# Kernel tuning notes

Hardware: AMD Instinct MI355X
Metric: run time of the kernel (lower is better)

## Reference

```python
import jax, jax.numpy as jnp
import numpy as np

MAX_DEPTH = 10
NUM_INPUT = 256
NUM_OUTPUT = 64
BATCH = 131072
N_INTERNAL = 2**MAX_DEPTH - 1  # 1023 heap-indexed internal nodes
N_LEAVES = 2**MAX_DEPTH        # 1024 leaves


def setup_inputs() -> dict:
    key = jax.random.key(0)
    k_x, k_w, k_b, k_a, k_l = jax.random.split(key, 5)
    x = jax.random.normal(k_x, (BATCH, NUM_INPUT), dtype=jnp.float32)
    # internal-node params (torch init: weights ~ N(0,0.1); bias/alpha zeros,
    # but we randomize bias/alpha so both branches are exercised)
    W = jax.random.normal(k_w, (N_INTERNAL, NUM_INPUT), dtype=jnp.float32) * 0.1
    b = jax.random.normal(k_b, (N_INTERNAL,), dtype=jnp.float32) * 0.1
    alpha = jax.random.normal(k_a, (N_INTERNAL,), dtype=jnp.float32)
    leaves = jax.random.normal(k_l, (N_LEAVES, NUM_OUTPUT), dtype=jnp.float32)
    return {"x": x, "W": W, "b": b, "alpha": alpha, "leaves": leaves}


def reference(x, W, b, alpha, leaves):
    # Batched hard root-to-leaf traversal of the soft binary tree.
    # Heap indexing: node i -> left child 2i+1, right child 2i+2.
    B = x.shape[0]
    idx = jnp.zeros((B,), dtype=jnp.int32)
    mult = jnp.ones((B,), dtype=x.dtype)
    for _ in range(MAX_DEPTH):  # fixed small structural loop over depth levels
        w = W[idx]  # [B, F] gather of per-node weights
        val = jax.nn.sigmoid(alpha[idx] * (jnp.einsum('bf,bf->b', x, w) + b[idx]))
        go_right = val >= 0.5
        # right branch contributes val, left branch contributes (1 - val)
        mult = mult * jnp.where(go_right, val, 1.0 - val)
        idx = 2 * idx + 1 + go_right.astype(jnp.int32)
    leaf_idx = idx - N_INTERNAL  # [B]
    return mult[:, None] * leaves[leaf_idx]  # [B, num_output]
```

## Files before the change

kernel.cpp:

```cpp
#include <hip/hip_runtime.h>

#define NUM_INPUT   256
#define NUM_OUTPUT  64
#define MAX_DEPTH   10
#define N_INTERNAL  1023
#define STAGED_NODES 31
#define STAGED_DEPTH 5
#define ELEMS_PER_WAVE 4
#define WAVES_PER_BLOCK 8
#define THREADS (WAVES_PER_BLOCK * 64)
#define ELEMS_PER_BLOCK (WAVES_PER_BLOCK * ELEMS_PER_WAVE)

__device__ __forceinline__ float group16_reduce_add(float acc) {
    int t;
    t = __builtin_amdgcn_update_dpp(0, __float_as_int(acc), 0x121, 0xf, 0xf, true);
    acc += __int_as_float(t);
    t = __builtin_amdgcn_update_dpp(0, __float_as_int(acc), 0x122, 0xf, 0xf, true);
    acc += __int_as_float(t);
    t = __builtin_amdgcn_update_dpp(0, __float_as_int(acc), 0x124, 0xf, 0xf, true);
    acc += __int_as_float(t);
    t = __builtin_amdgcn_update_dpp(0, __float_as_int(acc), 0x128, 0xf, 0xf, true);
    acc += __int_as_float(t);
    return acc;
}

__device__ __forceinline__ float group16_reduce_mul(float v) {
    int t;
    t = __builtin_amdgcn_update_dpp(0, __float_as_int(v), 0x121, 0xf, 0xf, true);
    v *= __int_as_float(t);
    t = __builtin_amdgcn_update_dpp(0, __float_as_int(v), 0x122, 0xf, 0xf, true);
    v *= __int_as_float(t);
    t = __builtin_amdgcn_update_dpp(0, __float_as_int(v), 0x124, 0xf, 0xf, true);
    v *= __int_as_float(t);
    t = __builtin_amdgcn_update_dpp(0, __float_as_int(v), 0x128, 0xf, 0xf, true);
    v *= __int_as_float(t);
    return v;
}

__global__ __launch_bounds__(THREADS, 8) void ogtree_kernel(
    const float* __restrict__ x,
    const float* __restrict__ W,
    const float* __restrict__ b,
    const float* __restrict__ alpha,
    const float* __restrict__ leaves,
    float* __restrict__ out)
{
    __shared__ float lds_w[STAGED_NODES * NUM_INPUT];
    __shared__ float lds_b[N_INTERNAL];
    __shared__ float lds_a[N_INTERNAL];

    const int tid  = threadIdx.x;
    const int lane = tid & 63;
    const int wid  = tid >> 6;
    const int g    = lane >> 4;
    const int s    = lane & 15;
    const int elem = blockIdx.x * ELEMS_PER_BLOCK + wid * ELEMS_PER_WAVE + g;

    const float4* xrow = reinterpret_cast<const float4*>(x + (size_t)elem * NUM_INPUT);
    float4 xv0 = xrow[0 * 16 + s];
    float4 xv1 = xrow[1 * 16 + s];
    float4 xv2 = xrow[2 * 16 + s];
    float4 xv3 = xrow[3 * 16 + s];

    {
        const float4* Wv = reinterpret_cast<const float4*>(W);
        float4* lw4 = reinterpret_cast<float4*>(lds_w);
        #pragma unroll
        for (int i = tid; i < STAGED_NODES * NUM_INPUT / 4; i += THREADS)
            lw4[i] = Wv[i];
        for (int i = tid; i < N_INTERNAL; i += THREADS) {
            lds_b[i] = b[i];
            lds_a[i] = alpha[i];
        }
    }
    __syncthreads();

    int   idx = 0;
    float zn[MAX_DEPTH];

    #define DEPTH_STEP(BASE, D)                                            \
    {                                                                      \
        const float4* wrow = reinterpret_cast<const float4*>(              \
            (BASE) + (size_t)idx * NUM_INPUT);                             \
        float a_i = lds_a[idx];                                            \
        float b_i = lds_b[idx];                                            \
        float4 w0 = wrow[0 * 16 + s];                                      \
        float4 w1 = wrow[1 * 16 + s];                                      \
        float4 w2 = wrow[2 * 16 + s];                                      \
        float4 w3 = wrow[3 * 16 + s];                                      \
        float acc0 = xv0.x * w0.x, acc1 = xv1.x * w1.x;                    \
        float acc2 = xv2.x * w2.x, acc3 = xv3.x * w3.x;                    \
        acc0 = fmaf(xv0.y, w0.y, acc0); acc1 = fmaf(xv1.y, w1.y, acc1);    \
        acc2 = fmaf(xv2.y, w2.y, acc2); acc3 = fmaf(xv3.y, w3.y, acc3);    \
        acc0 = fmaf(xv0.z, w0.z, acc0); acc1 = fmaf(xv1.z, w1.z, acc1);    \
        acc2 = fmaf(xv2.z, w2.z, acc2); acc3 = fmaf(xv3.z, w3.z, acc3);    \
        acc0 = fmaf(xv0.w, w0.w, acc0); acc1 = fmaf(xv1.w, w1.w, acc1);    \
        acc2 = fmaf(xv2.w, w2.w, acc2); acc3 = fmaf(xv3.w, w3.w, acc3);    \
        float acc = (acc0 + acc1) + (acc2 + acc3);                         \
        acc = group16_reduce_add(acc);                                     \
        float z = a_i * (acc + b_i);                                       \
        zn[D] = __int_as_float(__float_as_int(z) | 0x80000000);  \
        bool right = (z >= 0.0f);                                          \
        idx = 2 * idx + 1 + (right ? 1 : 0);                               \
    }

    #pragma unroll
    for (int d = 0; d < STAGED_DEPTH; ++d)
        DEPTH_STEP(lds_w, d);
    #pragma unroll
    for (int d = STAGED_DEPTH; d < MAX_DEPTH; ++d)
        DEPTH_STEP(W, d);
    #undef DEPTH_STEP

    float zsel = -1e30f;
    #pragma unroll
    for (int d = 0; d < MAX_DEPTH; ++d)
        zsel = (s == d) ? zn[d] : zsel;
    float f = 1.0f + __expf(zsel);
    float p = group16_reduce_mul(f);
    float mult = 1.0f / p;

    const int leaf = idx - N_INTERNAL;
    const float4 lv = reinterpret_cast<const float4*>(
        leaves + (size_t)leaf * NUM_OUTPUT)[s];
    float4 o;
    o.x = mult * lv.x;
    o.y = mult * lv.y;
    o.z = mult * lv.z;
    o.w = mult * lv.w;
    reinterpret_cast<float4*>(out + (size_t)elem * NUM_OUTPUT)[s] = o;
}

extern "C" void kernel_launch(void* const* d_in, const int* in_sizes, int n_in,
                              void* d_out, int out_size, void* d_ws, size_t ws_size,
                              hipStream_t stream) {
    const float* x      = (const float*)d_in[0];
    const float* W      = (const float*)d_in[1];
    const float* b      = (const float*)d_in[2];
    const float* alpha  = (const float*)d_in[3];
    const float* leaves = (const float*)d_in[4];
    float* out = (float*)d_out;

    const int batch  = in_sizes[0] / NUM_INPUT;
    const int blocks = batch / ELEMS_PER_BLOCK;

    ogtree_kernel<<<blocks, THREADS, 0, stream>>>(x, W, b, alpha, leaves, out);
}
```

Before: 49.42 us.

## Prefetch both child weight rows speculatively to hide global load latency

The global-memory depth levels now load the weight rows of both children of the current node while the current dot product is computed, then pick the correct one once the branch decision is known. The leaf rows for both final candidates are also fetched before the last decision. This takes the dependent global load off the critical path of each level, at the cost of twice the weight traffic and more registers. To make room for those registers the occupancy hint in launch bounds drops from 8 to 4.

```diff
diff --git a/kernel.cpp b/kernel.cpp
--- a/kernel.cpp
+++ b/kernel.cpp
@@ -37,7 +37,16 @@
     return v;
 }
 
-__global__ __launch_bounds__(THREADS, 8) void ogtree_kernel(
+__device__ __forceinline__ float4 sel4(bool c, float4 r, float4 l) {
+    float4 o;
+    o.x = c ? r.x : l.x;
+    o.y = c ? r.y : l.y;
+    o.z = c ? r.z : l.z;
+    o.w = c ? r.w : l.w;
+    return o;
+}
+
+__global__ __launch_bounds__(THREADS, 4) void ogtree_kernel(
     const float* __restrict__ x,
     const float* __restrict__ W,
     const float* __restrict__ b,
@@ -76,12 +85,13 @@
     __syncthreads();
 
     int   idx = 0;
+    bool  right;
     float zn[MAX_DEPTH];
 
-    #define DEPTH_STEP(BASE, D)                                            \
+    #define LDS_STEP(D)                                                    \
     {                                                                      \
         const float4* wrow = reinterpret_cast<const float4*>(              \
-            (BASE) + (size_t)idx * NUM_INPUT);                             \
+            lds_w + idx * NUM_INPUT);                                      \
         float a_i = lds_a[idx];                                            \
         float b_i = lds_b[idx];                                            \
         float4 w0 = wrow[0 * 16 + s];                                      \
@@ -100,17 +110,111 @@
         acc = group16_reduce_add(acc);                                     \
         float z = a_i * (acc + b_i);                                       \
         zn[D] = __int_as_float(__float_as_int(z) | 0x80000000);  \
-        bool right = (z >= 0.0f);                                          \
+        right = (z >= 0.0f);                                               \
         idx = 2 * idx + 1 + (right ? 1 : 0);                               \
     }
 
-    #pragma unroll
-    for (int d = 0; d < STAGED_DEPTH; ++d)
-        DEPTH_STEP(lds_w, d);
-    #pragma unroll
-    for (int d = STAGED_DEPTH; d < MAX_DEPTH; ++d)
-        DEPTH_STEP(W, d);
-    #undef DEPTH_STEP
+    LDS_STEP(0)
+    LDS_STEP(1)
+    LDS_STEP(2)
+    LDS_STEP(3)
+    #undef LDS_STEP
+
+    float4 wL0, wL1, wL2, wL3, wR0, wR1, wR2, wR3;
+
+    {
+        const float4* wrow = reinterpret_cast<const float4*>(lds_w + idx * NUM_INPUT);
+        float a_i = lds_a[idx];
+        float b_i = lds_b[idx];
+        float4 w0 = wrow[0 * 16 + s];
+        float4 w1 = wrow[1 * 16 + s];
+        float4 w2 = wrow[2 * 16 + s];
+        float4 w3 = wrow[3 * 16 + s];
+        const float4* pL = reinterpret_cast<const float4*>(W + (size_t)(2 * idx + 1) * NUM_INPUT);
+        const float4* pR = reinterpret_cast<const float4*>(W + (size_t)(2 * idx + 2) * NUM_INPUT);
+        wL0 = pL[0 * 16 + s]; wL1 = pL[1 * 16 + s];
+        wL2 = pL[2 * 16 + s]; wL3 = pL[3 * 16 + s];
+        wR0 = pR[0 * 16 + s]; wR1 = pR[1 * 16 + s];
+        wR2 = pR[2 * 16 + s]; wR3 = pR[3 * 16 + s];
+        float acc0 = xv0.x * w0.x, acc1 = xv1.x * w1.x;
+        float acc2 = xv2.x * w2.x, acc3 = xv3.x * w3.x;
+        acc0 = fmaf(xv0.y, w0.y, acc0); acc1 = fmaf(xv1.y, w1.y, acc1);
+        acc2 = fmaf(xv2.y, w2.y, acc2); acc3 = fmaf(xv3.y, w3.y, acc3);
+        acc0 = fmaf(xv0.z, w0.z, acc0); acc1 = fmaf(xv1.z, w1.z, acc1);
+        acc2 = fmaf(xv2.z, w2.z, acc2); acc3 = fmaf(xv3.z, w3.z, acc3);
+        acc0 = fmaf(xv0.w, w0.w, acc0); acc1 = fmaf(xv1.w, w1.w, acc1);
+        acc2 = fmaf(xv2.w, w2.w, acc2); acc3 = fmaf(xv3.w, w3.w, acc3);
+        float acc = (acc0 + acc1) + (acc2 + acc3);
+        acc = group16_reduce_add(acc);
+        float z = a_i * (acc + b_i);
+        zn[4] = __int_as_float(__float_as_int(z) | 0x80000000);
+        right = (z >= 0.0f);
+        idx = 2 * idx + 1 + (right ? 1 : 0);
+    }
+
+    #define GSTEP(D)                                                       \
+    {                                                                      \
+        float4 w0 = sel4(right, wR0, wL0);                                 \
+        float4 w1 = sel4(right, wR1, wL1);                                 \
+        float4 w2 = sel4(right, wR2, wL2);                                 \
+        float4 w3 = sel4(right, wR3, wL3);                                 \
+        float a_i = lds_a[idx];                                            \
+        float b_i = lds_b[idx];                                            \
+        const float4* pL = reinterpret_cast<const float4*>(                \
+            W + (size_t)(2 * idx + 1) * NUM_INPUT);                        \
+        const float4* pR = reinterpret_cast<const float4*>(                \
+            W + (size_t)(2 * idx + 2) * NUM_INPUT);                        \
+        wL0 = pL[0 * 16 + s]; wL1 = pL[1 * 16 + s];                        \
+        wL2 = pL[2 * 16 + s]; wL3 = pL[3 * 16 + s];                        \
+        wR0 = pR[0 * 16 + s]; wR1 = pR[1 * 16 + s];                        \
+        wR2 = pR[2 * 16 + s]; wR3 = pR[3 * 16 + s];                        \
+        float acc0 = xv0.x * w0.x, acc1 = xv1.x * w1.x;                    \
+        float acc2 = xv2.x * w2.x, acc3 = xv3.x * w3.x;                    \
+        acc0 = fmaf(xv0.y, w0.y, acc0); acc1 = fmaf(xv1.y, w1.y, acc1);    \
+        acc2 = fmaf(xv2.y, w2.y, acc2); acc3 = fmaf(xv3.y, w3.y, acc3);    \
+        acc0 = fmaf(xv0.z, w0.z, acc0); acc1 = fmaf(xv1.z, w1.z, acc1);    \
+        acc2 = fmaf(xv2.z, w2.z, acc2); acc3 = fmaf(xv3.z, w3.z, acc3);    \
+        acc0 = fmaf(xv0.w, w0.w, acc0); acc1 = fmaf(xv1.w, w1.w, acc1);    \
+        acc2 = fmaf(xv2.w, w2.w, acc2); acc3 = fmaf(xv3.w, w3.w, acc3);    \
+        float acc = (acc0 + acc1) + (acc2 + acc3);                         \
+        acc = group16_reduce_add(acc);                                     \
+        float z = a_i * (acc + b_i);                                       \
+        zn[D] = __int_as_float(__float_as_int(z) | 0x80000000);            \
+        right = (z >= 0.0f);                                               \
+        idx = 2 * idx + 1 + (right ? 1 : 0);                               \
+    }
+
+    GSTEP(5)
+    GSTEP(6)
+    GSTEP(7)
+    GSTEP(8)
+    #undef GSTEP
+
+    float4 lvL, lvR;
+    {
+        float4 w0 = sel4(right, wR0, wL0);
+        float4 w1 = sel4(right, wR1, wL1);
+        float4 w2 = sel4(right, wR2, wL2);
+        float4 w3 = sel4(right, wR3, wL3);
+        float a_i = lds_a[idx];
+        float b_i = lds_b[idx];
+        const int leafL = 2 * idx + 1 - N_INTERNAL;
+        lvL = reinterpret_cast<const float4*>(leaves + (size_t)leafL * NUM_OUTPUT)[s];
+        lvR = reinterpret_cast<const float4*>(leaves + (size_t)(leafL + 1) * NUM_OUTPUT)[s];
+        float acc0 = xv0.x * w0.x, acc1 = xv1.x * w1.x;
+        float acc2 = xv2.x * w2.x, acc3 = xv3.x * w3.x;
+        acc0 = fmaf(xv0.y, w0.y, acc0); acc1 = fmaf(xv1.y, w1.y, acc1);
+        acc2 = fmaf(xv2.y, w2.y, acc2); acc3 = fmaf(xv3.y, w3.y, acc3);
+        acc0 = fmaf(xv0.z, w0.z, acc0); acc1 = fmaf(xv1.z, w1.z, acc1);
+        acc2 = fmaf(xv2.z, w2.z, acc2); acc3 = fmaf(xv3.z, w3.z, acc3);
+        acc0 = fmaf(xv0.w, w0.w, acc0); acc1 = fmaf(xv1.w, w1.w, acc1);
+        acc2 = fmaf(xv2.w, w2.w, acc2); acc3 = fmaf(xv3.w, w3.w, acc3);
+        float acc = (acc0 + acc1) + (acc2 + acc3);
+        acc = group16_reduce_add(acc);
+        float z = a_i * (acc + b_i);
+        zn[9] = __int_as_float(__float_as_int(z) | 0x80000000);
+        right = (z >= 0.0f);
+    }
 
     float zsel = -1e30f;
     #pragma unroll
@@ -120,9 +224,7 @@
     float p = group16_reduce_mul(f);
     float mult = 1.0f / p;
 
-    const int leaf = idx - N_INTERNAL;
-    const float4 lv = reinterpret_cast<const float4*>(
-        leaves + (size_t)leaf * NUM_OUTPUT)[s];
+    const float4 lv = sel4(right, lvR, lvL);
     float4 o;
     o.x = mult * lv.x;
     o.y = mult * lv.y;
```

After: 66.02 us. +33.6%, slower.

## Split traversal into two phases with bucket sort by depth-5 node

Applied to the files above, without the earlier changes.

Splits the single traversal kernel into a pipeline. A first pass walks the top five levels from LDS and records each element's depth-5 node and partial product. Elements are then counting-sorted into 32 buckets by that node, and a second pass stages each bucket's 31-node subtree of W into LDS so the bottom five levels read from shared memory instead of gathering from global memory. In exchange it adds five kernel launches, rereads x a second time, and adds indirect scattered writes. A fallback monolithic kernel runs when the workspace is too small.

```diff
diff --git a/kernel.cpp b/kernel.cpp
--- a/kernel.cpp
+++ b/kernel.cpp
@@ -4,12 +4,7 @@
 #define NUM_OUTPUT  64
 #define MAX_DEPTH   10
 #define N_INTERNAL  1023
-#define STAGED_NODES 31
-#define STAGED_DEPTH 5
-#define ELEMS_PER_WAVE 4
-#define WAVES_PER_BLOCK 8
-#define THREADS (WAVES_PER_BLOCK * 64)
-#define ELEMS_PER_BLOCK (WAVES_PER_BLOCK * ELEMS_PER_WAVE)
+
 
 __device__ __forceinline__ float group16_reduce_add(float acc) {
     int t;
@@ -37,80 +32,240 @@
     return v;
 }
 
-__global__ __launch_bounds__(THREADS, 8) void ogtree_kernel(
-    const float* __restrict__ x,
-    const float* __restrict__ W,
-    const float* __restrict__ b,
-    const float* __restrict__ alpha,
-    const float* __restrict__ leaves,
-    float* __restrict__ out)
-{
-    __shared__ float lds_w[STAGED_NODES * NUM_INPUT];
-    __shared__ float lds_b[N_INTERNAL];
-    __shared__ float lds_a[N_INTERNAL];
+#define DOT16(WPTR, ACC)                                                    \
+    {                                                                       \
+        const float4* wr_ = reinterpret_cast<const float4*>(WPTR);          \
+        float4 w0 = wr_[s], w1 = wr_[16 + s], w2 = wr_[32 + s], w3 = wr_[48 + s]; \
+        float a0 = xv0.x * w0.x, a1 = xv1.x * w1.x;                         \
+        float a2 = xv2.x * w2.x, a3 = xv3.x * w3.x;                         \
+        a0 = fmaf(xv0.y, w0.y, a0); a1 = fmaf(xv1.y, w1.y, a1);             \
+        a2 = fmaf(xv2.y, w2.y, a2); a3 = fmaf(xv3.y, w3.y, a3);             \
+        a0 = fmaf(xv0.z, w0.z, a0); a1 = fmaf(xv1.z, w1.z, a1);             \
+        a2 = fmaf(xv2.z, w2.z, a2); a3 = fmaf(xv3.z, w3.z, a3);             \
+        a0 = fmaf(xv0.w, w0.w, a0); a1 = fmaf(xv1.w, w1.w, a1);             \
+        a2 = fmaf(xv2.w, w2.w, a2); a3 = fmaf(xv3.w, w3.w, a3);             \
+        ACC = group16_reduce_add((a0 + a1) + (a2 + a3));                    \
+    }
+
+#define TREE_STEP(WBASE, AARR, BARR, IDX, ZND)                              \
+    {                                                                       \
+        float a_i = (AARR)[IDX];                                            \
+        float b_i = (BARR)[IDX];                                            \
+        float acc_;                                                         \
+        DOT16((WBASE) + (size_t)(IDX) * NUM_INPUT, acc_);                   \
+        float z = a_i * (acc_ + b_i);                                       \
+        ZND = __int_as_float(__float_as_int(z) | 0x80000000);               \
+        IDX = 2 * (IDX) + 1 + ((z >= 0.0f) ? 1 : 0);                        \
+    }
+
+#define P1_THREADS 1024
+#define P1_ELEMS   64
+
+__global__ __launch_bounds__(P1_THREADS) void ogtree_p1(
+    const float* __restrict__ x, const float* __restrict__ W,
+    const float* __restrict__ b, const float* __restrict__ alpha,
+    int* __restrict__ cnt, int* __restrict__ idx5a, float* __restrict__ p5a)
+{
+    __shared__ float lds_w[31 * NUM_INPUT];
+    __shared__ float la[31], lb_[31];
+    __shared__ int   h[32];
 
     const int tid  = threadIdx.x;
-    const int lane = tid & 63;
-    const int wid  = tid >> 6;
-    const int g    = lane >> 4;
-    const int s    = lane & 15;
-    const int elem = blockIdx.x * ELEMS_PER_BLOCK + wid * ELEMS_PER_WAVE + g;
+    const int lane = tid & 63, wid = tid >> 6;
+    const int g    = lane >> 4, s = lane & 15;
+    const int elem = blockIdx.x * P1_ELEMS + wid * 4 + g;
 
     const float4* xrow = reinterpret_cast<const float4*>(x + (size_t)elem * NUM_INPUT);
-    float4 xv0 = xrow[0 * 16 + s];
-    float4 xv1 = xrow[1 * 16 + s];
-    float4 xv2 = xrow[2 * 16 + s];
-    float4 xv3 = xrow[3 * 16 + s];
+    float4 xv0 = xrow[s], xv1 = xrow[16 + s], xv2 = xrow[32 + s], xv3 = xrow[48 + s];
 
     {
         const float4* Wv = reinterpret_cast<const float4*>(W);
         float4* lw4 = reinterpret_cast<float4*>(lds_w);
         #pragma unroll
-        for (int i = tid; i < STAGED_NODES * NUM_INPUT / 4; i += THREADS)
-            lw4[i] = Wv[i];
-        for (int i = tid; i < N_INTERNAL; i += THREADS) {
-            lds_b[i] = b[i];
-            lds_a[i] = alpha[i];
+        for (int i = tid; i < 31 * 64; i += P1_THREADS) lw4[i] = Wv[i];
+        if (tid < 31) { la[tid] = alpha[tid]; lb_[tid] = b[tid]; }
+        if (tid < 32) h[tid] = 0;
+    }
+    __syncthreads();
+
+    int idx = 0;
+    float zn[5];
+    #pragma unroll
+    for (int d = 0; d < 5; ++d)
+        TREE_STEP(lds_w, la, lb_, idx, zn[d]);
+
+    float zsel = -1e30f;
+    #pragma unroll
+    for (int d = 0; d < 5; ++d)
+        zsel = (s == d) ? zn[d] : zsel;
+    float f = 1.0f + __expf(zsel);
+    float p = group16_reduce_mul(f);
+
+    if (s == 0) {
+        idx5a[elem] = idx;
+        p5a[elem]   = p;
+        atomicAdd(&h[idx - 31], 1);
+    }
+    __syncthreads();
+    if (tid < 32 && h[tid] > 0) atomicAdd(&cnt[tid], h[tid]);
+}
+
+__global__ void ogtree_scan(const int* __restrict__ cnt, int* __restrict__ cur)
+{
+    if (threadIdx.x == 0) {
+        int acc = 0;
+        for (int i = 0; i < 32; ++i) { cur[i] = acc; acc += cnt[i]; }
+    }
+}
+
+__global__ void ogtree_zero(int* __restrict__ cnt)
+{
+    if (threadIdx.x < 32) cnt[threadIdx.x] = 0;
+}
+
+#define SC_THREADS 256
+__global__ __launch_bounds__(SC_THREADS) void ogtree_scatter(
+    const int* __restrict__ idx5a, int* __restrict__ cur, int* __restrict__ ids)
+{
+    __shared__ int h[32], base[32];
+    const int tid = threadIdx.x;
+    const int e   = blockIdx.x * SC_THREADS + tid;
+    if (tid < 32) h[tid] = 0;
+    __syncthreads();
+    const int bkt  = idx5a[e] - 31;
+    const int rank = atomicAdd(&h[bkt], 1);
+    __syncthreads();
+    if (tid < 32 && h[tid] > 0) base[tid] = atomicAdd(&cur[tid], h[tid]);
+    __syncthreads();
+    ids[base[bkt] + rank] = e;
+}
+
+#define P2_THREADS 1024
+#define P2_ELEMS   64
+
+__global__ __launch_bounds__(P2_THREADS) void ogtree_p2(
+    const float* __restrict__ x, const float* __restrict__ W,
+    const float* __restrict__ b, const float* __restrict__ alpha,
+    const float* __restrict__ leaves,
+    const int* __restrict__ ids, const int* __restrict__ idx5a,
+    const float* __restrict__ p5a, float* __restrict__ out)
+{
+    __shared__ float lsub[31 * NUM_INPUT];
+    __shared__ float la[31], lb_[31];
+    __shared__ int   s_n5, s_uni;
+
+    const int tid  = threadIdx.x;
+    const int lane = tid & 63, wid = tid >> 6;
+    const int g    = lane >> 4, s = lane & 15;
+    const int i0   = blockIdx.x * P2_ELEMS;
+
+    const int   id   = ids[i0 + wid * 4 + g];
+    const int   myn5 = idx5a[id];
+    const float p5v  = p5a[id];
+
+    const float4* xrow = reinterpret_cast<const float4*>(x + (size_t)id * NUM_INPUT);
+    float4 xv0 = xrow[s], xv1 = xrow[16 + s], xv2 = xrow[32 + s], xv3 = xrow[48 + s];
+
+    if (tid == 0) {
+        int na = idx5a[ids[i0]];
+        int nb = idx5a[ids[i0 + P2_ELEMS - 1]];
+        s_n5  = na;
+        s_uni = (na == nb);
+    }
+    __syncthreads();
+    const bool uni = (s_uni != 0);
+    const int  n5  = s_n5;
+
+    if (uni) {
+        const float4* Wv = reinterpret_cast<const float4*>(W);
+        float4* ls4 = reinterpret_cast<float4*>(lsub);
+        #pragma unroll
+        for (int i = tid; i < 31 * 64; i += P2_THREADS) {
+            int row = i >> 6;
+            int col = i & 63;
+            int lvl = 31 - __clz(row + 1);
+            int gl  = ((n5 + 1) << lvl) - 1 + (row + 1 - (1 << lvl));
+            ls4[row * 64 + col] = Wv[(size_t)gl * 64 + col];
         }
-    }
-    __syncthreads();
-
-    int   idx = 0;
+        if (tid < 31) {
+            int lvl = 31 - __clz(tid + 1);
+            int gl  = ((n5 + 1) << lvl) - 1 + (tid + 1 - (1 << lvl));
+            la[tid]  = alpha[gl];
+            lb_[tid] = b[gl];
+        }
+    }
+    __syncthreads();
+
+    float zn[5];
+    int leaf;
+    if (uni) {
+        int li = 0;
+        #pragma unroll
+        for (int d = 0; d < 5; ++d)
+            TREE_STEP(lsub, la, lb_, li, zn[d]);
+        leaf = (((n5 + 1) << 5) - 1 + (li - 31)) - N_INTERNAL;
+    } else {
+        int idxg = myn5;
+        #pragma unroll
+        for (int d = 0; d < 5; ++d)
+            TREE_STEP(W, alpha, b, idxg, zn[d]);
+        leaf = idxg - N_INTERNAL;
+    }
+
+    float zsel = -1e30f;
+    #pragma unroll
+    for (int d = 0; d < 5; ++d)
+        zsel = (s == d) ? zn[d] : zsel;
+    float f = 1.0f + __expf(zsel);
+    float p = group16_reduce_mul(f);
+    float mult = 1.0f / (p * p5v);
+
+    const float4 lv = reinterpret_cast<const float4*>(
+        leaves + (size_t)leaf * NUM_OUTPUT)[s];
+    float4 o;
+    o.x = mult * lv.x;
+    o.y = mult * lv.y;
+    o.z = mult * lv.z;
+    o.w = mult * lv.w;
+    reinterpret_cast<float4*>(out + (size_t)id * NUM_OUTPUT)[s] = o;
+}
+
+#define MONO_THREADS 512
+#define MONO_ELEMS   32
+
+__global__ __launch_bounds__(MONO_THREADS) void ogtree_mono(
+    const float* __restrict__ x, const float* __restrict__ W,
+    const float* __restrict__ b, const float* __restrict__ alpha,
+    const float* __restrict__ leaves, float* __restrict__ out)
+{
+    __shared__ float lds_w[31 * NUM_INPUT];
+    __shared__ float la[31], lb_[31];
+
+    const int tid  = threadIdx.x;
+    const int lane = tid & 63, wid = tid >> 6;
+    const int g    = lane >> 4, s = lane & 15;
+    const int elem = blockIdx.x * MONO_ELEMS + wid * 4 + g;
+
+    const float4* xrow = reinterpret_cast<const float4*>(x + (size_t)elem * NUM_INPUT);
+    float4 xv0 = xrow[s], xv1 = xrow[16 + s], xv2 = xrow[32 + s], xv3 = xrow[48 + s];
+
+    {
+        const float4* Wv = reinterpret_cast<const float4*>(W);
+        float4* lw4 = reinterpret_cast<float4*>(lds_w);
+        #pragma unroll
+        for (int i = tid; i < 31 * 64; i += MONO_THREADS) lw4[i] = Wv[i];
+        if (tid < 31) { la[tid] = alpha[tid]; lb_[tid] = b[tid]; }
+    }
+    __syncthreads();
+
+    int idx = 0;
     float zn[MAX_DEPTH];
-
-    #define DEPTH_STEP(BASE, D)                                            \
-    {                                                                      \
-        const float4* wrow = reinterpret_cast<const float4*>(              \
-            (BASE) + (size_t)idx * NUM_INPUT);                             \
-        float a_i = lds_a[idx];                                            \
-        float b_i = lds_b[idx];                                            \
-        float4 w0 = wrow[0 * 16 + s];                                      \
-        float4 w1 = wrow[1 * 16 + s];                                      \
-        float4 w2 = wrow[2 * 16 + s];                                      \
-        float4 w3 = wrow[3 * 16 + s];                                      \
-        float acc0 = xv0.x * w0.x, acc1 = xv1.x * w1.x;                    \
-        float acc2 = xv2.x * w2.x, acc3 = xv3.x * w3.x;                    \
-        acc0 = fmaf(xv0.y, w0.y, acc0); acc1 = fmaf(xv1.y, w1.y, acc1);    \
-        acc2 = fmaf(xv2.y, w2.y, acc2); acc3 = fmaf(xv3.y, w3.y, acc3);    \
-        acc0 = fmaf(xv0.z, w0.z, acc0); acc1 = fmaf(xv1.z, w1.z, acc1);    \
-        acc2 = fmaf(xv2.z, w2.z, acc2); acc3 = fmaf(xv3.z, w3.z, acc3);    \
-        acc0 = fmaf(xv0.w, w0.w, acc0); acc1 = fmaf(xv1.w, w1.w, acc1);    \
-        acc2 = fmaf(xv2.w, w2.w, acc2); acc3 = fmaf(xv3.w, w3.w, acc3);    \
-        float acc = (acc0 + acc1) + (acc2 + acc3);                         \
-        acc = group16_reduce_add(acc);                                     \
-        float z = a_i * (acc + b_i);                                       \
-        zn[D] = __int_as_float(__float_as_int(z) | 0x80000000);  \
-        bool right = (z >= 0.0f);                                          \
-        idx = 2 * idx + 1 + (right ? 1 : 0);                               \
-    }
-
-    #pragma unroll
-    for (int d = 0; d < STAGED_DEPTH; ++d)
-        DEPTH_STEP(lds_w, d);
-    #pragma unroll
-    for (int d = STAGED_DEPTH; d < MAX_DEPTH; ++d)
-        DEPTH_STEP(W, d);
-    #undef DEPTH_STEP
+    #pragma unroll
+    for (int d = 0; d < 5; ++d)
+        TREE_STEP(lds_w, la, lb_, idx, zn[d]);
+    #pragma unroll
+    for (int d = 5; d < MAX_DEPTH; ++d)
+        TREE_STEP(W, alpha, b, idx, zn[d]);
 
     float zsel = -1e30f;
     #pragma unroll
@@ -141,8 +296,26 @@
     const float* leaves = (const float*)d_in[4];
     float* out = (float*)d_out;
 
-    const int batch  = in_sizes[0] / NUM_INPUT;
-    const int blocks = batch / ELEMS_PER_BLOCK;
-
-    ogtree_kernel<<<blocks, THREADS, 0, stream>>>(x, W, b, alpha, leaves, out);
-}
+    const int batch = in_sizes[0] / NUM_INPUT;
+
+    const size_t need = 64 * sizeof(int) + (size_t)batch * 4 * 3;
+    if (ws_size < need) {
+        ogtree_mono<<<batch / MONO_ELEMS, MONO_THREADS, 0, stream>>>(
+            x, W, b, alpha, leaves, out);
+        return;
+    }
+
+    int*   cnt   = (int*)d_ws;
+    int*   cur   = cnt + 32;
+    int*   idx5a = cnt + 64;
+    float* p5a   = (float*)(idx5a + batch);
+    int*   ids   = (int*)(p5a + batch);
+
+    ogtree_zero<<<1, 64, 0, stream>>>(cnt);
+    ogtree_p1<<<batch / P1_ELEMS, P1_THREADS, 0, stream>>>(
+        x, W, b, alpha, cnt, idx5a, p5a);
+    ogtree_scan<<<1, 64, 0, stream>>>(cnt, cur);
+    ogtree_scatter<<<batch / SC_THREADS, SC_THREADS, 0, stream>>>(idx5a, cur, ids);
+    ogtree_p2<<<batch / P2_ELEMS, P2_THREADS, 0, stream>>>(
+        x, W, b, alpha, leaves, ids, idx5a, p5a, out);
+}
```

Result: slower. 91.44 us (+85.0%).

## Process four elements per group with software-prefetched x rows

Applied to the files above, without the earlier changes.

Each 16-lane group now handles four batch elements in sequence instead of one. The grid shrinks to a fixed 1024 blocks, so the LDS staging of the top tree levels is amortised over more elements. The next element's x row is prefetched into a second register set while the global-memory levels of the current element run, hiding load latency. This adds register pressure (launch bounds lowered to 4 waves/SIMD) and hardcodes the grid size to the test batch.

```diff
diff --git a/kernel.cpp b/kernel.cpp
--- a/kernel.cpp
+++ b/kernel.cpp
@@ -5,11 +5,9 @@
 #define MAX_DEPTH   10
 #define N_INTERNAL  1023
 #define STAGED_NODES 31
-#define STAGED_DEPTH 5
-#define ELEMS_PER_WAVE 4
-#define WAVES_PER_BLOCK 8
-#define THREADS (WAVES_PER_BLOCK * 64)
-#define ELEMS_PER_BLOCK (WAVES_PER_BLOCK * ELEMS_PER_WAVE)
+#define THREADS 512
+#define NBLOCKS 1024
+#define ELEMS_PER_GROUP 4
 
 __device__ __forceinline__ float group16_reduce_add(float acc) {
     int t;
@@ -37,7 +35,71 @@
     return v;
 }
 
-__global__ __launch_bounds__(THREADS, 8) void ogtree_kernel(
+#define STEP_X(BASE, IDX, ZND, X0, X1, X2, X3)                              \
+    {                                                                       \
+        float a_i = lds_a[IDX];                                             \
+        float b_i = lds_b[IDX];                                             \
+        const float4* wr_ = reinterpret_cast<const float4*>(                \
+            (BASE) + (size_t)(IDX) * NUM_INPUT);                            \
+        float4 w0 = wr_[s], w1 = wr_[16 + s], w2 = wr_[32 + s], w3 = wr_[48 + s]; \
+        float a0 = X0.x * w0.x, a1 = X1.x * w1.x;                           \
+        float a2 = X2.x * w2.x, a3 = X3.x * w3.x;                           \
+        a0 = fmaf(X0.y, w0.y, a0); a1 = fmaf(X1.y, w1.y, a1);               \
+        a2 = fmaf(X2.y, w2.y, a2); a3 = fmaf(X3.y, w3.y, a3);               \
+        a0 = fmaf(X0.z, w0.z, a0); a1 = fmaf(X1.z, w1.z, a1);               \
+        a2 = fmaf(X2.z, w2.z, a2); a3 = fmaf(X3.z, w3.z, a3);               \
+        a0 = fmaf(X0.w, w0.w, a0); a1 = fmaf(X1.w, w1.w, a1);               \
+        a2 = fmaf(X2.w, w2.w, a2); a3 = fmaf(X3.w, w3.w, a3);               \
+        float acc_ = group16_reduce_add((a0 + a1) + (a2 + a3));             \
+        float z = a_i * (acc_ + b_i);                                       \
+        ZND = __int_as_float(__float_as_int(z) | 0x80000000);               \
+        IDX = 2 * (IDX) + 1 + ((z >= 0.0f) ? 1 : 0);                        \
+    }
+
+#define ONE_ELEM(E, XC0, XC1, XC2, XC3, XN0, XN1, XN2, XN3, PF)             \
+    {                                                                       \
+        int idx = 0;                                                        \
+        float zn0, zn1, zn2, zn3, zn4, zn5, zn6, zn7, zn8, zn9;             \
+                                        \
+        STEP_X(lds_w, idx, zn0, XC0, XC1, XC2, XC3)                         \
+        STEP_X(lds_w, idx, zn1, XC0, XC1, XC2, XC3)                         \
+        STEP_X(lds_w, idx, zn2, XC0, XC1, XC2, XC3)                         \
+        STEP_X(lds_w, idx, zn3, XC0, XC1, XC2, XC3)                         \
+        STEP_X(lds_w, idx, zn4, XC0, XC1, XC2, XC3)                         \
+        if (PF) {                                                           \
+            const float4* xp_ = reinterpret_cast<const float4*>(            \
+                x + (size_t)(gbase + 4 * ((E) + 1)) * NUM_INPUT);           \
+            XN0 = xp_[s];      XN1 = xp_[16 + s];                           \
+            XN2 = xp_[32 + s]; XN3 = xp_[48 + s];                           \
+            __builtin_amdgcn_sched_barrier(0);                              \
+        }                                                                   \
+           \
+        STEP_X(W, idx, zn5, XC0, XC1, XC2, XC3)                             \
+        STEP_X(W, idx, zn6, XC0, XC1, XC2, XC3)                             \
+        STEP_X(W, idx, zn7, XC0, XC1, XC2, XC3)                             \
+        STEP_X(W, idx, zn8, XC0, XC1, XC2, XC3)                             \
+        STEP_X(W, idx, zn9, XC0, XC1, XC2, XC3)                             \
+                 \
+        float zsel = -1e30f;                                                \
+        zsel = (s == 0) ? zn0 : zsel; zsel = (s == 1) ? zn1 : zsel;         \
+        zsel = (s == 2) ? zn2 : zsel; zsel = (s == 3) ? zn3 : zsel;         \
+        zsel = (s == 4) ? zn4 : zsel; zsel = (s == 5) ? zn5 : zsel;         \
+        zsel = (s == 6) ? zn6 : zsel; zsel = (s == 7) ? zn7 : zsel;         \
+        zsel = (s == 8) ? zn8 : zsel; zsel = (s == 9) ? zn9 : zsel;         \
+        float f = 1.0f + __expf(zsel);                                      \
+        float p = group16_reduce_mul(f);                                    \
+        float mult = 1.0f / p;                                              \
+        const int leaf = idx - N_INTERNAL;                                  \
+        const float4 lv = reinterpret_cast<const float4*>(                  \
+            leaves + (size_t)leaf * NUM_OUTPUT)[s];                         \
+        float4 o;                                                           \
+        o.x = mult * lv.x; o.y = mult * lv.y;                               \
+        o.z = mult * lv.z; o.w = mult * lv.w;                               \
+        reinterpret_cast<float4*>(                                          \
+            out + (size_t)(gbase + 4 * (E)) * NUM_OUTPUT)[s] = o;           \
+    }
+
+__global__ __launch_bounds__(THREADS, 4) void ogtree_kernel(
     const float* __restrict__ x,
     const float* __restrict__ W,
     const float* __restrict__ b,
@@ -54,13 +116,10 @@
     const int wid  = tid >> 6;
     const int g    = lane >> 4;
     const int s    = lane & 15;
-    const int elem = blockIdx.x * ELEMS_PER_BLOCK + wid * ELEMS_PER_WAVE + g;
+    const int gbase = blockIdx.x * (THREADS / 64) * 16 + wid * 16 + g;
 
-    const float4* xrow = reinterpret_cast<const float4*>(x + (size_t)elem * NUM_INPUT);
-    float4 xv0 = xrow[0 * 16 + s];
-    float4 xv1 = xrow[1 * 16 + s];
-    float4 xv2 = xrow[2 * 16 + s];
-    float4 xv3 = xrow[3 * 16 + s];
+    const float4* xp0 = reinterpret_cast<const float4*>(x + (size_t)gbase * NUM_INPUT);
+    float4 xa0 = xp0[s], xa1 = xp0[16 + s], xa2 = xp0[32 + s], xa3 = xp0[48 + s];
 
     {
         const float4* Wv = reinterpret_cast<const float4*>(W);
@@ -75,60 +134,12 @@
     }
     __syncthreads();
 
-    int   idx = 0;
-    float zn[MAX_DEPTH];
+    float4 xb0, xb1, xb2, xb3;
 
-    #define DEPTH_STEP(BASE, D)                                            \
-    {                                                                      \
-        const float4* wrow = reinterpret_cast<const float4*>(              \
-            (BASE) + (size_t)idx * NUM_INPUT);                             \
-        float a_i = lds_a[idx];                                            \
-        float b_i = lds_b[idx];                                            \
-        float4 w0 = wrow[0 * 16 + s];                                      \
-        float4 w1 = wrow[1 * 16 + s];                                      \
-        float4 w2 = wrow[2 * 16 + s];                                      \
-        float4 w3 = wrow[3 * 16 + s];                                      \
-        float acc0 = xv0.x * w0.x, acc1 = xv1.x * w1.x;                    \
-        float acc2 = xv2.x * w2.x, acc3 = xv3.x * w3.x;                    \
-        acc0 = fmaf(xv0.y, w0.y, acc0); acc1 = fmaf(xv1.y, w1.y, acc1);    \
-        acc2 = fmaf(xv2.y, w2.y, acc2); acc3 = fmaf(xv3.y, w3.y, acc3);    \
-        acc0 = fmaf(xv0.z, w0.z, acc0); acc1 = fmaf(xv1.z, w1.z, acc1);    \
-        acc2 = fmaf(xv2.z, w2.z, acc2); acc3 = fmaf(xv3.z, w3.z, acc3);    \
-        acc0 = fmaf(xv0.w, w0.w, acc0); acc1 = fmaf(xv1.w, w1.w, acc1);    \
-        acc2 = fmaf(xv2.w, w2.w, acc2); acc3 = fmaf(xv3.w, w3.w, acc3);    \
-        float acc = (acc0 + acc1) + (acc2 + acc3);                         \
-        acc = group16_reduce_add(acc);                                     \
-        float z = a_i * (acc + b_i);                                       \
-        zn[D] = __int_as_float(__float_as_int(z) | 0x80000000);  \
-        bool right = (z >= 0.0f);                                          \
-        idx = 2 * idx + 1 + (right ? 1 : 0);                               \
-    }
-
-    #pragma unroll
-    for (int d = 0; d < STAGED_DEPTH; ++d)
-        DEPTH_STEP(lds_w, d);
-    #pragma unroll
-    for (int d = STAGED_DEPTH; d < MAX_DEPTH; ++d)
-        DEPTH_STEP(W, d);
-    #undef DEPTH_STEP
-
-    float zsel = -1e30f;
-    #pragma unroll
-    for (int d = 0; d < MAX_DEPTH; ++d)
-        zsel = (s == d) ? zn[d] : zsel;
-    float f = 1.0f + __expf(zsel);
-    float p = group16_reduce_mul(f);
-    float mult = 1.0f / p;
-
-    const int leaf = idx - N_INTERNAL;
-    const float4 lv = reinterpret_cast<const float4*>(
-        leaves + (size_t)leaf * NUM_OUTPUT)[s];
-    float4 o;
-    o.x = mult * lv.x;
-    o.y = mult * lv.y;
-    o.z = mult * lv.z;
-    o.w = mult * lv.w;
-    reinterpret_cast<float4*>(out + (size_t)elem * NUM_OUTPUT)[s] = o;
+    ONE_ELEM(0, xa0, xa1, xa2, xa3, xb0, xb1, xb2, xb3, 1)
+    ONE_ELEM(1, xb0, xb1, xb2, xb3, xa0, xa1, xa2, xa3, 1)
+    ONE_ELEM(2, xa0, xa1, xa2, xa3, xb0, xb1, xb2, xb3, 1)
+    ONE_ELEM(3, xb0, xb1, xb2, xb3, xa0, xa1, xa2, xa3, 0)
 }
 
 extern "C" void kernel_launch(void* const* d_in, const int* in_sizes, int n_in,
@@ -141,8 +152,5 @@
     const float* leaves = (const float*)d_in[4];
     float* out = (float*)d_out;
 
-    const int batch  = in_sizes[0] / NUM_INPUT;
-    const int blocks = batch / ELEMS_PER_BLOCK;
-
-    ogtree_kernel<<<blocks, THREADS, 0, stream>>>(x, W, b, alpha, leaves, out);
+    ogtree_kernel<<<NBLOCKS, THREADS, 0, stream>>>(x, W, b, alpha, leaves, out);
 }
```

Result: faster. 47.14 us (median of 2 runs) (-4.6%).
